# Performance work log

Measured on AMD Instinct MI355X. Metric: run time of the kernel, lower is better.

Reference implementation:

```python
import math
import jax, jax.numpy as jnp
import numpy as np

B, S, D, H = 8, 4096, 1024, 16
HD = D // H  # head_dim = 64


def setup_inputs() -> dict:
    key = jax.random.key(0)
    ks = jax.random.split(key, 13)
    sc = 1.0 / math.sqrt(D)
    scd = 1.0 / math.sqrt(HD)
    return {
        "X":   jax.random.normal(ks[0], (B, S, D), jnp.float32),
        "Wq":  jax.random.normal(ks[1], (D, D), jnp.float32) * sc,
        "bq":  jax.random.normal(ks[2], (D,), jnp.float32) * 0.01,
        "Wk":  jax.random.normal(ks[3], (D, D), jnp.float32) * sc,
        "bk":  jax.random.normal(ks[4], (D,), jnp.float32) * 0.01,
        "Wv":  jax.random.normal(ks[5], (D, D), jnp.float32) * sc,
        "bv":  jax.random.normal(ks[6], (D,), jnp.float32) * 0.01,
        "wql": jax.random.normal(ks[7], (HD,), jnp.float32) * scd,
        "bql": jax.random.normal(ks[8], (1,), jnp.float32) * 0.01,
        "wkl": jax.random.normal(ks[9], (HD,), jnp.float32) * scd,
        "bkl": jax.random.normal(ks[10], (1,), jnp.float32) * 0.01,
        "Wr":  jax.random.normal(ks[11], (HD, HD), jnp.float32) * scd,
        "br":  jax.random.normal(ks[12], (HD,), jnp.float32) * 0.01,
    }


def _split_heads(t):
    b, s, d = t.shape
    return t.reshape(b, s, H, HD).transpose(0, 2, 1, 3)  # b h s d


def reference(X, Wq, bq, Wk, bk, Wv, bv, wql, bql, wkl, bkl, Wr, br):
    inv_sqrt_d = 1.0 / math.sqrt(HD)
    q = _split_heads(X @ Wq + bq)  # [b,h,s,d]
    k = _split_heads(X @ Wk + bk)
    v = _split_heads(X @ Wv + bv)

    # query pooling: softmax over seq of a scalar logit per position
    alphas = jax.nn.softmax((jnp.einsum('bhsd,d->bhs', q, wql) + bql[0]) * inv_sqrt_d, axis=-1)
    global_query = jnp.einsum('bhs,bhsd->bhd', alphas, q)[:, :, None, :]  # [b,h,1,d]

    p = k * global_query  # elementwise gating, [b,h,s,d]
    betas = jax.nn.softmax((jnp.einsum('bhsd,d->bhs', p, wkl) + bkl[0]) * inv_sqrt_d, axis=-1)
    global_key = jnp.einsum('bhs,bhsd->bhd', betas, p)[:, :, None, :]  # [b,h,1,d]

    u = v * global_key  # [b,h,s,d]
    out = q + (u @ Wr + br)  # residual + tiny head_dim projection (dropout=0)
    b, h, s, d = out.shape
    return out.transpose(0, 2, 1, 3).reshape(b, s, h * d)
```

## Files before the change

### kernel.cpp

```cpp
#include <hip/hip_runtime.h>
#include <stdint.h>

#define B_   8
#define S_   4096
#define D_   1024
#define H_   16
#define HD_  64
#define M_   (B_ * S_)
#define N3   (3 * D_)

using f32x4 = __attribute__((ext_vector_type(4))) float;
using s8v   = __attribute__((ext_vector_type(8))) short;
using u16x8 = __attribute__((ext_vector_type(8))) unsigned short;
using bf8v  = __attribute__((ext_vector_type(8))) __bf16;

static __device__ __forceinline__ float bf2f(unsigned short u) {
  union { unsigned int i; float f; } x; x.i = ((unsigned int)u) << 16; return x.f;
}
static __device__ __forceinline__ unsigned short f2bf(float f) {
  union { float f; unsigned int i; } x; x.f = f;
  unsigned int r = x.i + 0x7fffu + ((x.i >> 16) & 1u);
  return (unsigned short)(r >> 16);
}

template <typename T>
static __device__ __forceinline__ auto mfma_try(T a, T b, f32x4 c, int)
    -> decltype(__builtin_amdgcn_mfma_f32_16x16x32_bf16(a, b, c, 0, 0, 0)) {
  return __builtin_amdgcn_mfma_f32_16x16x32_bf16(a, b, c, 0, 0, 0);
}
template <typename T>
static __device__ __forceinline__ f32x4 mfma_try(T a, T b, f32x4 c, long) {
  return __builtin_amdgcn_mfma_f32_16x16x32_bf16(
      __builtin_bit_cast(bf8v, a), __builtin_bit_cast(bf8v, b), c, 0, 0, 0);
}
static __device__ __forceinline__ f32x4 mfma_bf16(s8v a, s8v b, f32x4 c) {
  return mfma_try(a, b, c, 0);
}

static __device__ __forceinline__ void gl_lds16(const void* g, void* l) {
  __builtin_amdgcn_global_load_lds(
      (const __attribute__((address_space(1))) void*)g,
      (__attribute__((address_space(3))) void*)l, 16, 0, 0);
}

__global__ __launch_bounds__(256) void cvt_bf16_k(const float* __restrict__ in,
                                                  unsigned short* __restrict__ out) {
  size_t i = ((size_t)blockIdx.x * 256 + threadIdx.x) * 8;
  f32x4 a = *(const f32x4*)(in + i);
  f32x4 b = *(const f32x4*)(in + i + 4);
  u16x8 o;
#pragma unroll
  for (int j = 0; j < 4; ++j) { o[j] = f2bf(a[j]); o[4 + j] = f2bf(b[j]); }
  *(u16x8*)(out + i) = o;
}

__global__ __launch_bounds__(256) void packWT_k(const float* __restrict__ Wq,
                                                const float* __restrict__ Wk,
                                                const float* __restrict__ Wv,
                                                unsigned short* __restrict__ WT) {
  __shared__ unsigned short tile[64][65];
  const float* W = blockIdx.z == 0 ? Wq : (blockIdx.z == 1 ? Wk : Wv);
  unsigned short* O = WT + (size_t)blockIdx.z * 1024 * 1024;
  const int tk = blockIdx.x * 64, tn = blockIdx.y * 64;
  const int t = threadIdx.x;
#pragma unroll
  for (int i = 0; i < 16; ++i) {
    int idx = i * 256 + t; int r = idx >> 6, c = idx & 63;
    tile[c][r] = f2bf(W[(size_t)(tk + r) * 1024 + tn + c]);
  }
  __syncthreads();
#pragma unroll
  for (int i = 0; i < 16; ++i) {
    int idx = i * 256 + t; int r = idx >> 6, c = idx & 63;
    O[(size_t)(tn + r) * 1024 + tk + c] = tile[r][c];
  }
}

__global__ void packbias_k(const float* __restrict__ bq, const float* __restrict__ bk,
                           const float* __restrict__ bv, float* __restrict__ bcat) {
  int i = blockIdx.x * 256 + threadIdx.x;
  if (i < 1024) bcat[i] = bq[i];
  else if (i < 2048) bcat[i] = bk[i - 1024];
  else if (i < 3072) bcat[i] = bv[i - 2048];
}

__global__ __launch_bounds__(256) void gemm_qkv(const unsigned short* __restrict__ A,
                                                const unsigned short* __restrict__ BT,
                                                const float* __restrict__ bias,
                                                unsigned short* __restrict__ C) {
  __shared__ unsigned short As[128 * 64];
  __shared__ unsigned short Bs[128 * 64];
  const int t = threadIdx.x;
  const int w = t >> 6, l = t & 63;
  const int mrow0 = blockIdx.y * 128;
  const int ncol0 = blockIdx.x * 128;
  const int srow = t >> 3;
  const int scol = (t & 7) * 8;
  const unsigned short* Ag = A + (size_t)(mrow0 + srow) * 1024 + scol;
  const unsigned short* Bg = BT + (size_t)(ncol0 + srow) * 1024 + scol;
  unsigned short* Al = &As[srow * 64 + scol];
  unsigned short* Bl = &Bs[srow * 64 + scol];

  f32x4 acc[4][4];
#pragma unroll
  for (int m = 0; m < 4; ++m)
#pragma unroll
    for (int n = 0; n < 4; ++n) acc[m][n] = f32x4{0.f, 0.f, 0.f, 0.f};

  const int wr = (w >> 1) * 64, wc = (w & 1) * 64;
  const int fr = l & 15, fk = (l >> 4) * 8;

  for (int kt = 0; kt < 16; ++kt) {
    const int kk = kt * 64;
#pragma unroll
    for (int i = 0; i < 4; ++i) {
      gl_lds16(Ag + (size_t)(i * 32) * 1024 + kk, Al + i * 32 * 64);
      gl_lds16(Bg + (size_t)(i * 32) * 1024 + kk, Bl + i * 32 * 64);
    }
    __syncthreads();
#pragma unroll
    for (int ks = 0; ks < 2; ++ks) {
      s8v af[4], bf[4];
#pragma unroll
      for (int m = 0; m < 4; ++m)
        af[m] = *(const s8v*)&As[(wr + m * 16 + fr) * 64 + ks * 32 + fk];
#pragma unroll
      for (int n = 0; n < 4; ++n)
        bf[n] = *(const s8v*)&Bs[(wc + n * 16 + fr) * 64 + ks * 32 + fk];
#pragma unroll
      for (int m = 0; m < 4; ++m)
#pragma unroll
        for (int n = 0; n < 4; ++n)
          acc[m][n] = mfma_bf16(af[m], bf[n], acc[m][n]);
    }
    __syncthreads();
  }
  const int r4 = (l >> 4) * 4;
#pragma unroll
  for (int n = 0; n < 4; ++n) {
    const int gc = ncol0 + wc + n * 16 + fr;
    const float bb = bias[gc];
#pragma unroll
    for (int m = 0; m < 4; ++m)
#pragma unroll
      for (int i = 0; i < 4; ++i) {
        const int gr = mrow0 + wr + m * 16 + r4 + i;
        C[(size_t)gr * N3 + gc] = f2bf(acc[m][n][i] + bb);
      }
  }
}

template <int GATED>
__global__ __launch_bounds__(256) void plog_k(const unsigned short* __restrict__ QKV,
                                              const float* __restrict__ wvec,
                                              const float* __restrict__ bias,
                                              float* __restrict__ L, int off) {
  const int t = threadIdx.x;
  const int rg = blockIdx.x * 4 + (t >> 6);
  const int l = t & 63;
  const size_t base = (size_t)rg * N3 + off;
  u16x8 v0 = *(const u16x8*)(QKV + base + l * 16);
  u16x8 v1 = *(const u16x8*)(QKV + base + l * 16 + 8);
  const int h = l >> 2;
  const float* w;
  if (GATED) w = wvec + (((size_t)(rg >> 12) * 16 + h) * 64) + (l & 3) * 16;
  else       w = wvec + (l & 3) * 16;
  float d = 0.f;
#pragma unroll
  for (int j = 0; j < 8; ++j) d += bf2f(v0[j]) * w[j];
#pragma unroll
  for (int j = 0; j < 8; ++j) d += bf2f(v1[j]) * w[8 + j];
  d += __shfl_xor(d, 1); d += __shfl_xor(d, 2);
  if ((l & 3) == 0) L[(size_t)rg * 16 + h] = (d + bias[0]) * 0.125f;
}

__global__ __launch_bounds__(256) void pstats_k(const float* __restrict__ L,
                                                float* __restrict__ stats) {
  __shared__ float redm[4], reds[4];
  const int t = threadIdx.x;
  const int bh = blockIdx.x;
  const int b = bh >> 4, h = bh & 15;
  float vals[16];
  float mx = -1e30f;
#pragma unroll
  for (int j = 0; j < 16; ++j) {
    vals[j] = L[((size_t)b * S_ + t + j * 256) * 16 + h];
    mx = fmaxf(mx, vals[j]);
  }
  for (int off = 32; off; off >>= 1) mx = fmaxf(mx, __shfl_xor(mx, off));
  if ((t & 63) == 0) redm[t >> 6] = mx;
  __syncthreads();
  mx = fmaxf(fmaxf(redm[0], redm[1]), fmaxf(redm[2], redm[3]));
  float sm = 0.f;
#pragma unroll
  for (int j = 0; j < 16; ++j) sm += expf(vals[j] - mx);
  for (int off = 32; off; off >>= 1) sm += __shfl_xor(sm, off);
  if ((t & 63) == 0) reds[t >> 6] = sm;
  __syncthreads();
  if (t == 0) {
    stats[bh * 2] = mx;
    stats[bh * 2 + 1] = 1.f / (reds[0] + reds[1] + reds[2] + reds[3]);
  }
}

__global__ __launch_bounds__(256) void psum_k(const unsigned short* __restrict__ QKV,
                                              const float* __restrict__ L,
                                              const float* __restrict__ stats,
                                              float* __restrict__ pg, int off) {
  __shared__ float red2[256];
  const int t = threadIdx.x;
  const int c = blockIdx.x, bh = blockIdx.y;
  const int b = bh >> 4, h = bh & 15;
  const float MX = stats[bh * 2], INV = stats[bh * 2 + 1];
  const int w = t >> 6, d = t & 63;
  float acc = 0.f;
  const int s0 = c * 256 + w * 64;
#pragma unroll 4
  for (int i = 0; i < 64; ++i) {
    const size_t row = (size_t)b * S_ + s0 + i;
    const float a = expf(L[row * 16 + h] - MX) * INV;
    acc += a * bf2f(QKV[row * N3 + off + h * 64 + d]);
  }
  red2[t] = acc;
  __syncthreads();
  if (t < 64)
    pg[((size_t)bh * 16 + c) * 64 + t] =
        red2[t] + red2[64 + t] + red2[128 + t] + red2[192 + t];
}

__global__ __launch_bounds__(256) void predq_k(const float* __restrict__ pg,
                                               const float* __restrict__ wkl,
                                               float* __restrict__ gq,
                                               float* __restrict__ weffK) {
  const int idx = blockIdx.x * 256 + threadIdx.x;
  const int bh = idx >> 6, d = idx & 63;
  float s = 0.f;
#pragma unroll
  for (int c = 0; c < 16; ++c) s += pg[((size_t)bh * 16 + c) * 64 + d];
  gq[idx] = s;
  weffK[idx] = s * wkl[d];
}

__global__ __launch_bounds__(256) void predk_k(const float* __restrict__ pg,
                                               const float* __restrict__ gq,
                                               float* __restrict__ gk) {
  const int idx = blockIdx.x * 256 + threadIdx.x;
  const int bh = idx >> 6, d = idx & 63;
  float s = 0.f;
#pragma unroll
  for (int c = 0; c < 16; ++c) s += pg[((size_t)bh * 16 + c) * 64 + d];
  gk[idx] = gq[idx] * s;
}

__global__ __launch_bounds__(256) void final_out(const unsigned short* __restrict__ QKV,
                                                 const float* __restrict__ gk,
                                                 const float* __restrict__ Wr,
                                                 const float* __restrict__ br,
                                                 float* __restrict__ out) {
  __shared__ unsigned short Us[128 * 64];
  __shared__ float wrs[64 * 64];
  __shared__ float gks[64];
  const int t = threadIdx.x;
  const int w = t >> 6, l = t & 63;
  const int bh = blockIdx.y, sc = blockIdx.x;
  const int b = bh >> 4, h = bh & 15;
  const int s0 = sc * 128;
  if (t < 64) gks[t] = gk[bh * 64 + t];
#pragma unroll
  for (int i = 0; i < 16; ++i) wrs[i * 256 + t] = Wr[i * 256 + t];
  __syncthreads();
  const int rsub = t >> 3, csub = (t & 7) * 8;
  const size_t vbase = (((size_t)b * S_ + s0) * N3) + 2048 + h * 64;
#pragma unroll
  for (int i = 0; i < 4; ++i) {
    int r = i * 32 + rsub;
    u16x8 v = *(const u16x8*)(QKV + vbase + (size_t)r * N3 + csub);
    u16x8 u;
#pragma unroll
    for (int j = 0; j < 8; ++j) u[j] = f2bf(bf2f(v[j]) * gks[csub + j]);
    *(u16x8*)&Us[r * 64 + csub] = u;
  }
  const int fr = l & 15, fk = (l >> 4) * 8;
  s8v bfrag[2][4];
#pragma unroll
  for (int ks = 0; ks < 2; ++ks)
#pragma unroll
    for (int nf = 0; nf < 4; ++nf) {
      s8v tmp;
#pragma unroll
      for (int j = 0; j < 8; ++j)
        tmp[j] = (short)f2bf(wrs[(ks * 32 + fk + j) * 64 + nf * 16 + fr]);
      bfrag[ks][nf] = tmp;
    }
  __syncthreads();
  f32x4 acc[2][4];
#pragma unroll
  for (int rf = 0; rf < 2; ++rf)
#pragma unroll
    for (int nf = 0; nf < 4; ++nf) acc[rf][nf] = f32x4{0.f, 0.f, 0.f, 0.f};
#pragma unroll
  for (int ks = 0; ks < 2; ++ks) {
    s8v af[2];
#pragma unroll
    for (int rf = 0; rf < 2; ++rf)
      af[rf] = *(const s8v*)&Us[(w * 32 + rf * 16 + fr) * 64 + ks * 32 + fk];
#pragma unroll
    for (int rf = 0; rf < 2; ++rf)
#pragma unroll
      for (int nf = 0; nf < 4; ++nf)
        acc[rf][nf] = mfma_bf16(af[rf], bfrag[ks][nf], acc[rf][nf]);
  }
  const int r4 = (l >> 4) * 4;
#pragma unroll
  for (int rf = 0; rf < 2; ++rf)
#pragma unroll
    for (int nf = 0; nf < 4; ++nf)
#pragma unroll
      for (int i = 0; i < 4; ++i) {
        int srow = s0 + w * 32 + rf * 16 + r4 + i;
        int dcol = nf * 16 + fr;
        size_t row = (size_t)b * S_ + srow;
        float q = bf2f(QKV[row * N3 + h * 64 + dcol]);
        out[row * 1024 + h * 64 + dcol] = q + acc[rf][nf][i] + br[dcol];
      }
}

extern "C" void kernel_launch(void* const* d_in, const int* in_sizes, int n_in,
                              void* d_out, int out_size, void* d_ws, size_t ws_size,
                              hipStream_t stream) {
  const float* X   = (const float*)d_in[0];
  const float* Wq  = (const float*)d_in[1];
  const float* bq  = (const float*)d_in[2];
  const float* Wk  = (const float*)d_in[3];
  const float* bk  = (const float*)d_in[4];
  const float* Wv  = (const float*)d_in[5];
  const float* bv  = (const float*)d_in[6];
  const float* wql = (const float*)d_in[7];
  const float* bql = (const float*)d_in[8];
  const float* wkl = (const float*)d_in[9];
  const float* bkl = (const float*)d_in[10];
  const float* Wr  = (const float*)d_in[11];
  const float* br  = (const float*)d_in[12];
  float* out = (float*)d_out;

  char* ws = (char*)d_ws;
  unsigned short* Xb  = (unsigned short*)ws;
  unsigned short* WT  = (unsigned short*)(ws + 67108864);
  float* bcat         = (float*)(ws + 73400320);
  unsigned short* QKV = (unsigned short*)(ws + 73412608);
  float* Lq    = (float*)(ws + 0);
  float* Lk    = (float*)(ws + 2097152);
  float* pgq   = (float*)(ws + 4194304);
  float* pgk   = (float*)(ws + 4718592);
  float* statsQ= (float*)(ws + 5242880);
  float* statsK= (float*)(ws + 5246976);
  float* gq    = (float*)(ws + 6291456);
  float* weffK = (float*)(ws + 6324224);
  float* gk    = (float*)(ws + 6356992);

  hipLaunchKernelGGL(cvt_bf16_k, dim3(16384), dim3(256), 0, stream, X, Xb);
  hipLaunchKernelGGL(packWT_k, dim3(16, 16, 3), dim3(256), 0, stream, Wq, Wk, Wv, WT);
  hipLaunchKernelGGL(packbias_k, dim3(12), dim3(256), 0, stream, bq, bk, bv, bcat);
  hipLaunchKernelGGL(gemm_qkv, dim3(24, 256), dim3(256), 0, stream, Xb, WT, bcat, QKV);

  hipLaunchKernelGGL((plog_k<0>), dim3(8192), dim3(256), 0, stream, QKV, wql, bql, Lq, 0);
  hipLaunchKernelGGL(pstats_k, dim3(128), dim3(256), 0, stream, Lq, statsQ);
  hipLaunchKernelGGL(psum_k, dim3(16, 128), dim3(256), 0, stream, QKV, Lq, statsQ, pgq, 0);
  hipLaunchKernelGGL(predq_k, dim3(32), dim3(256), 0, stream, pgq, wkl, gq, weffK);
  hipLaunchKernelGGL((plog_k<1>), dim3(8192), dim3(256), 0, stream, QKV, weffK, bkl, Lk, 1024);
  hipLaunchKernelGGL(pstats_k, dim3(128), dim3(256), 0, stream, Lk, statsK);
  hipLaunchKernelGGL(psum_k, dim3(16, 128), dim3(256), 0, stream, QKV, Lk, statsK, pgk, 1024);
  hipLaunchKernelGGL(predk_k, dim3(32), dim3(256), 0, stream, pgk, gq, gk);

  hipLaunchKernelGGL(final_out, dim3(32, 128), dim3(256), 0, stream, QKV, gk, Wr, br, out);
}
```

Measured before the change: 659.1 us.

## Replace QKV GEMM with 256x256-tile double-buffered pipelined kernel

Swaps the 128x128-tile QKV GEMM for a 512-thread kernel that computes 256x256 tiles. It double-buffers 128KB of dynamic LDS so the next k-tile's global-to-LDS loads overlap the MFMA work, and uses an XOR swizzle to avoid LDS bank conflicts. It also remaps block IDs for better L2 locality and raises wave priority around the MFMAs. The aim is to raise arithmetic intensity and hide load latency, at the cost of more registers and LDS per block, which limits occupancy to one block per CU (128KB of 160KB), and more delicate hand-placed waitcnt/barrier synchronisation.

```diff
diff --git a/kernel.cpp b/kernel.cpp
--- a/kernel.cpp
+++ b/kernel.cpp
@@ -84,67 +84,116 @@
   else if (i < 3072) bcat[i] = bv[i - 2048];
 }
 
-__global__ __launch_bounds__(256) void gemm_qkv(const unsigned short* __restrict__ A,
-                                                const unsigned short* __restrict__ BT,
-                                                const float* __restrict__ bias,
-                                                unsigned short* __restrict__ C) {
-  __shared__ unsigned short As[128 * 64];
-  __shared__ unsigned short Bs[128 * 64];
+static __device__ __forceinline__ void stage_half(const unsigned short* __restrict__ g,
+                                                  int grow0, int ktile, int kh,
+                                                  char* lds_region, int t) {
+#pragma unroll
+  for (int j = 0; j < 2; ++j) {
+    const int li = j * 512 + t;
+    const int row = li >> 2, p = li & 3;
+    const int sg = kh * 4 + (p ^ (row & 3));
+    const unsigned short* src = g + (size_t)(grow0 + row) * 1024 + ktile * 64 + sg * 8;
+    gl_lds16(src, lds_region + kh * 16384 + li * 16);
+  }
+}
+
+__global__ __launch_bounds__(512, 2) void gemm256(const unsigned short* __restrict__ A,
+                                                  const unsigned short* __restrict__ BT,
+                                                  const float* __restrict__ bias,
+                                                  unsigned short* __restrict__ C) {
+  extern __shared__ char smem[];
   const int t = threadIdx.x;
   const int w = t >> 6, l = t & 63;
-  const int mrow0 = blockIdx.y * 128;
-  const int ncol0 = blockIdx.x * 128;
-  const int srow = t >> 3;
-  const int scol = (t & 7) * 8;
-  const unsigned short* Ag = A + (size_t)(mrow0 + srow) * 1024 + scol;
-  const unsigned short* Bg = BT + (size_t)(ncol0 + srow) * 1024 + scol;
-  unsigned short* Al = &As[srow * 64 + scol];
-  unsigned short* Bl = &Bs[srow * 64 + scol];
-
-  f32x4 acc[4][4];
-#pragma unroll
-  for (int m = 0; m < 4; ++m)
+  int bid = blockIdx.x;
+  const int cpx = gridDim.x >> 3;
+  bid = (bid & 7) * cpx + (bid >> 3);
+  const int by = bid & 127;
+  const int bx = bid >> 7;
+  const int mrow0 = by * 256, ncol0 = bx * 256;
+  const int wr = w >> 2, wc = w & 3;
+  const int fr = l & 15;
+  const int p_read = (((l >> 4) ^ (fr & 3)) << 4);
+
+  f32x4 acc[8][4];
+#pragma unroll
+  for (int m = 0; m < 8; ++m)
 #pragma unroll
     for (int n = 0; n < 4; ++n) acc[m][n] = f32x4{0.f, 0.f, 0.f, 0.f};
 
-  const int wr = (w >> 1) * 64, wc = (w & 1) * 64;
-  const int fr = l & 15, fk = (l >> 4) * 8;
-
-  for (int kt = 0; kt < 16; ++kt) {
-    const int kk = kt * 64;
-#pragma unroll
-    for (int i = 0; i < 4; ++i) {
-      gl_lds16(Ag + (size_t)(i * 32) * 1024 + kk, Al + i * 32 * 64);
-      gl_lds16(Bg + (size_t)(i * 32) * 1024 + kk, Bl + i * 32 * 64);
+  stage_half(A,  mrow0, 0, 0, smem, t);
+  stage_half(BT, ncol0, 0, 0, smem + 32768, t);
+  stage_half(A,  mrow0, 0, 1, smem, t);
+  stage_half(BT, ncol0, 0, 1, smem + 32768, t);
+  asm volatile("s_waitcnt vmcnt(4)" ::: "memory");
+  __builtin_amdgcn_s_barrier();
+  __builtin_amdgcn_sched_barrier(0);
+
+  const int arow = wr * 128 + fr;
+  const int brow = wc * 64 + fr;
+
+  for (int kt = 0; kt < 15; ++kt) {
+    const int base_rd = (kt & 1) * 65536;
+    const int base_wr = base_rd ^ 65536;
+#pragma unroll
+    for (int kk = 0; kk < 2; ++kk) {
+      s8v af[8], bfv[4];
+#pragma unroll
+      for (int m = 0; m < 8; ++m)
+        af[m] = *(const s8v*)(smem + base_rd + kk * 16384 + (arow + m * 16) * 64 + p_read);
+#pragma unroll
+      for (int n = 0; n < 4; ++n)
+        bfv[n] = *(const s8v*)(smem + base_rd + 32768 + kk * 16384 + (brow + n * 16) * 64 + p_read);
+      stage_half(A,  mrow0, kt + 1, kk, smem + base_wr, t);
+      stage_half(BT, ncol0, kt + 1, kk, smem + base_wr + 32768, t);
+      __builtin_amdgcn_s_setprio(1);
+#pragma unroll
+      for (int m = 0; m < 8; ++m)
+#pragma unroll
+        for (int n = 0; n < 4; ++n)
+          acc[m][n] = mfma_bf16(af[m], bfv[n], acc[m][n]);
+      __builtin_amdgcn_s_setprio(0);
+      __builtin_amdgcn_sched_barrier(0);
+      asm volatile("s_waitcnt vmcnt(4)" ::: "memory");
+      __builtin_amdgcn_s_barrier();
+      __builtin_amdgcn_sched_barrier(0);
     }
-    __syncthreads();
-#pragma unroll
-    for (int ks = 0; ks < 2; ++ks) {
-      s8v af[4], bf[4];
-#pragma unroll
-      for (int m = 0; m < 4; ++m)
-        af[m] = *(const s8v*)&As[(wr + m * 16 + fr) * 64 + ks * 32 + fk];
+  }
+  {
+    const int base_rd = 65536;
+#pragma unroll
+    for (int kk = 0; kk < 2; ++kk) {
+      s8v af[8], bfv[4];
+#pragma unroll
+      for (int m = 0; m < 8; ++m)
+        af[m] = *(const s8v*)(smem + base_rd + kk * 16384 + (arow + m * 16) * 64 + p_read);
 #pragma unroll
       for (int n = 0; n < 4; ++n)
-        bf[n] = *(const s8v*)&Bs[(wc + n * 16 + fr) * 64 + ks * 32 + fk];
-#pragma unroll
-      for (int m = 0; m < 4; ++m)
+        bfv[n] = *(const s8v*)(smem + base_rd + 32768 + kk * 16384 + (brow + n * 16) * 64 + p_read);
+      __builtin_amdgcn_s_setprio(1);
+#pragma unroll
+      for (int m = 0; m < 8; ++m)
 #pragma unroll
         for (int n = 0; n < 4; ++n)
-          acc[m][n] = mfma_bf16(af[m], bf[n], acc[m][n]);
+          acc[m][n] = mfma_bf16(af[m], bfv[n], acc[m][n]);
+      __builtin_amdgcn_s_setprio(0);
+      if (kk == 0) {
+        __builtin_amdgcn_sched_barrier(0);
+        asm volatile("s_waitcnt vmcnt(0)" ::: "memory");
+        __builtin_amdgcn_s_barrier();
+        __builtin_amdgcn_sched_barrier(0);
+      }
     }
-    __syncthreads();
   }
   const int r4 = (l >> 4) * 4;
 #pragma unroll
   for (int n = 0; n < 4; ++n) {
-    const int gc = ncol0 + wc + n * 16 + fr;
+    const int gc = ncol0 + wc * 64 + n * 16 + fr;
     const float bb = bias[gc];
 #pragma unroll
-    for (int m = 0; m < 4; ++m)
+    for (int m = 0; m < 8; ++m)
 #pragma unroll
       for (int i = 0; i < 4; ++i) {
-        const int gr = mrow0 + wr + m * 16 + r4 + i;
+        const int gr = mrow0 + wr * 128 + m * 16 + r4 + i;
         C[(size_t)gr * N3 + gc] = f2bf(acc[m][n][i] + bb);
       }
   }
@@ -358,10 +407,13 @@
   float* weffK = (float*)(ws + 6324224);
   float* gk    = (float*)(ws + 6356992);
 
+  hipFuncSetAttribute(reinterpret_cast<const void*>(gemm256),
+                      hipFuncAttributeMaxDynamicSharedMemorySize, 131072);
+
   hipLaunchKernelGGL(cvt_bf16_k, dim3(16384), dim3(256), 0, stream, X, Xb);
   hipLaunchKernelGGL(packWT_k, dim3(16, 16, 3), dim3(256), 0, stream, Wq, Wk, Wv, WT);
   hipLaunchKernelGGL(packbias_k, dim3(12), dim3(256), 0, stream, bq, bk, bv, bcat);
-  hipLaunchKernelGGL(gemm_qkv, dim3(24, 256), dim3(256), 0, stream, Xb, WT, bcat, QKV);
+  hipLaunchKernelGGL(gemm256, dim3(1536), dim3(512), 131072, stream, Xb, WT, bcat, QKV);
 
   hipLaunchKernelGGL((plog_k<0>), dim3(8192), dim3(256), 0, stream, QKV, wql, bql, Lq, 0);
   hipLaunchKernelGGL(pstats_k, dim3(128), dim3(256), 0, stream, Lq, statsQ);
```

New measurement: 624.0 us. 5.3% less time.

## Rewrite QKV GEMM as double-buffered 256x256 tile kernel and fuse softmax stats

Applied to the files above, without the earlier changes.

Replaces the 128x128 single-buffered QKV GEMM with a 256x256-tile, 512-thread kernel. It double-buffers 128 KB of dynamic LDS, interleaves global-to-LDS staging with MFMA quarter-steps using vmcnt waits and barriers, and remaps block IDs so neighbouring blocks reuse tiles in cache. The aim is to hide memory latency and raise data reuse in the dominant GEMM. Separately, the pstats kernel is folded into psum, so each psum block recomputes the softmax max and sum itself and two launches disappear, at the cost of redundant reduction work.

```diff
diff --git a/kernel.cpp b/kernel.cpp
--- a/kernel.cpp
+++ b/kernel.cpp
@@ -84,70 +84,130 @@
   else if (i < 3072) bcat[i] = bv[i - 2048];
 }
 
-__global__ __launch_bounds__(256) void gemm_qkv(const unsigned short* __restrict__ A,
-                                                const unsigned short* __restrict__ BT,
-                                                const float* __restrict__ bias,
-                                                unsigned short* __restrict__ C) {
-  __shared__ unsigned short As[128 * 64];
-  __shared__ unsigned short Bs[128 * 64];
+static __device__ __forceinline__ void stage_half(const unsigned short* __restrict__ g,
+                                                  int grow0, int kt, int h,
+                                                  char* region, int t) {
+#pragma unroll
+  for (int j = 0; j < 2; ++j) {
+    const int li = j * 512 + t;
+    const int kh = li >> 9, idx = li & 511;
+    const int row = h * 128 + (idx >> 2), slot = idx & 3;
+    const unsigned short* src = g + (size_t)(grow0 + row) * 1024 + kt * 64 + kh * 32 + slot * 8;
+    gl_lds16(src, region + kh * 16384 + h * 8192 + idx * 16);
+  }
+}
+
+#define VMCNT(n) asm volatile("s_waitcnt vmcnt(" #n ")" ::: "memory")
+#define BAR()    { __builtin_amdgcn_s_barrier(); __builtin_amdgcn_sched_barrier(0); }
+
+__global__ __launch_bounds__(512, 2) void gemm256(const unsigned short* __restrict__ A,
+                                                  const unsigned short* __restrict__ BT,
+                                                  const float* __restrict__ bias,
+                                                  unsigned short* __restrict__ C) {
+  extern __shared__ char smem[];
   const int t = threadIdx.x;
   const int w = t >> 6, l = t & 63;
-  const int mrow0 = blockIdx.y * 128;
-  const int ncol0 = blockIdx.x * 128;
-  const int srow = t >> 3;
-  const int scol = (t & 7) * 8;
-  const unsigned short* Ag = A + (size_t)(mrow0 + srow) * 1024 + scol;
-  const unsigned short* Bg = BT + (size_t)(ncol0 + srow) * 1024 + scol;
-  unsigned short* Al = &As[srow * 64 + scol];
-  unsigned short* Bl = &Bs[srow * 64 + scol];
-
-  f32x4 acc[4][4];
-#pragma unroll
-  for (int m = 0; m < 4; ++m)
+  const int cpx = gridDim.x >> 3;
+  const int lid = ((int)blockIdx.x & 7) * cpx + ((int)blockIdx.x >> 3);
+  const int by = lid / 12, bx = lid - by * 12;
+  const int mrow0 = by * 256, ncol0 = bx * 256;
+  const int wr = w >> 2, wc = w & 3;
+  const int fr = l & 15;
+  const int pr = (l >> 4) * 16;
+  const int arow0 = wr * 64 + fr;
+  const int brow0 = wc * 32 + fr;
+
+  f32x4 acc[8][4];
+#pragma unroll
+  for (int m = 0; m < 8; ++m)
 #pragma unroll
     for (int n = 0; n < 4; ++n) acc[m][n] = f32x4{0.f, 0.f, 0.f, 0.f};
 
-  const int wr = (w >> 1) * 64, wc = (w & 1) * 64;
-  const int fr = l & 15, fk = (l >> 4) * 8;
-
-  for (int kt = 0; kt < 16; ++kt) {
-    const int kk = kt * 64;
-#pragma unroll
-    for (int i = 0; i < 4; ++i) {
-      gl_lds16(Ag + (size_t)(i * 32) * 1024 + kk, Al + i * 32 * 64);
-      gl_lds16(Bg + (size_t)(i * 32) * 1024 + kk, Bl + i * 32 * 64);
-    }
-    __syncthreads();
-#pragma unroll
-    for (int ks = 0; ks < 2; ++ks) {
-      s8v af[4], bf[4];
-#pragma unroll
-      for (int m = 0; m < 4; ++m)
-        af[m] = *(const s8v*)&As[(wr + m * 16 + fr) * 64 + ks * 32 + fk];
-#pragma unroll
-      for (int n = 0; n < 4; ++n)
-        bf[n] = *(const s8v*)&Bs[(wc + n * 16 + fr) * 64 + ks * 32 + fk];
-#pragma unroll
-      for (int m = 0; m < 4; ++m)
-#pragma unroll
-        for (int n = 0; n < 4; ++n)
-          acc[m][n] = mfma_bf16(af[m], bf[n], acc[m][n]);
-    }
-    __syncthreads();
+  stage_half(A,  mrow0, 0, 0, smem, t);
+  stage_half(BT, ncol0, 0, 0, smem + 32768, t);
+  stage_half(BT, ncol0, 0, 1, smem + 32768, t);
+  stage_half(A,  mrow0, 0, 1, smem, t);
+  VMCNT(4);
+  BAR();
+
+  s8v a0[8], a1[8], b0[4], b1[4];
+
+#define RD_A(dst, MH, bufp)                                                        \
+  _Pragma("unroll") for (int mf = 0; mf < 4; ++mf)                                 \
+  _Pragma("unroll") for (int ks = 0; ks < 2; ++ks)                                 \
+    dst[mf * 2 + ks] = *(const s8v*)((bufp) + ks * 16384 +                         \
+                        ((MH) * 128 + arow0 + mf * 16) * 64 + pr);
+#define RD_B(dst, NH, bufp)                                                        \
+  _Pragma("unroll") for (int nf = 0; nf < 2; ++nf)                                 \
+  _Pragma("unroll") for (int ks = 0; ks < 2; ++ks)                                 \
+    dst[nf * 2 + ks] = *(const s8v*)((bufp) + 32768 + ks * 16384 +                 \
+                        ((NH) * 128 + brow0 + nf * 16) * 64 + pr);
+#define MFMA_Q(av, bv, MH, NH)                                                     \
+  __builtin_amdgcn_s_setprio(1);                                                   \
+  _Pragma("unroll") for (int mf = 0; mf < 4; ++mf)                                 \
+  _Pragma("unroll") for (int nf = 0; nf < 2; ++nf)                                 \
+  _Pragma("unroll") for (int ks = 0; ks < 2; ++ks)                                 \
+    acc[(MH) * 4 + mf][(NH) * 2 + nf] =                                            \
+        mfma_bf16(av[mf * 2 + ks], bv[nf * 2 + ks], acc[(MH) * 4 + mf][(NH) * 2 + nf]); \
+  __builtin_amdgcn_s_setprio(0);                                                   \
+  __builtin_amdgcn_sched_barrier(0);
+
+  for (int kt = 0; kt < 15; ++kt) {
+    char* buf  = smem + (kt & 1) * 65536;
+    char* nbuf = smem + ((kt + 1) & 1) * 65536;
+    RD_A(a0, 0, buf); RD_B(b0, 0, buf);
+    stage_half(A, mrow0, kt + 1, 0, nbuf, t);
+    BAR();
+    MFMA_Q(a0, b0, 0, 0);
+    VMCNT(4); BAR();
+    RD_B(b1, 1, buf);
+    stage_half(BT, ncol0, kt + 1, 0, nbuf + 32768, t);
+    BAR();
+    MFMA_Q(a0, b1, 0, 1);
+    VMCNT(4); BAR();
+    RD_A(a1, 1, buf);
+    stage_half(BT, ncol0, kt + 1, 1, nbuf + 32768, t);
+    BAR();
+    MFMA_Q(a1, b1, 1, 1);
+    VMCNT(4); BAR();
+    stage_half(A, mrow0, kt + 1, 1, nbuf, t);
+    BAR();
+    MFMA_Q(a1, b0, 1, 0);
+    VMCNT(4); BAR();
+  }
+  {
+    char* buf = smem + 65536;
+    RD_A(a0, 0, buf); RD_B(b0, 0, buf);
+    BAR();
+    MFMA_Q(a0, b0, 0, 0);
+    VMCNT(2); BAR();
+    RD_B(b1, 1, buf);
+    BAR();
+    MFMA_Q(a0, b1, 0, 1);
+    VMCNT(0); BAR();
+    RD_A(a1, 1, buf);
+    MFMA_Q(a1, b1, 1, 1);
+    MFMA_Q(a1, b0, 1, 0);
   }
   const int r4 = (l >> 4) * 4;
 #pragma unroll
-  for (int n = 0; n < 4; ++n) {
-    const int gc = ncol0 + wc + n * 16 + fr;
-    const float bb = bias[gc];
-#pragma unroll
-    for (int m = 0; m < 4; ++m)
-#pragma unroll
-      for (int i = 0; i < 4; ++i) {
-        const int gr = mrow0 + wr + m * 16 + r4 + i;
-        C[(size_t)gr * N3 + gc] = f2bf(acc[m][n][i] + bb);
-      }
-  }
+  for (int mh = 0; mh < 2; ++mh)
+#pragma unroll
+    for (int mf = 0; mf < 4; ++mf)
+#pragma unroll
+      for (int nh = 0; nh < 2; ++nh)
+#pragma unroll
+        for (int nf = 0; nf < 2; ++nf) {
+          const int gc = ncol0 + nh * 128 + wc * 32 + nf * 16 + fr;
+          const int grb = mrow0 + mh * 128 + wr * 64 + mf * 16 + r4;
+          const float bb = bias[gc];
+#pragma unroll
+          for (int i = 0; i < 4; ++i)
+            C[(size_t)(grb + i) * N3 + gc] = f2bf(acc[mh * 4 + mf][nh * 2 + nf][i] + bb);
+        }
+#undef RD_A
+#undef RD_B
+#undef MFMA_Q
 }
 
 template <int GATED>
@@ -174,11 +234,12 @@
   if ((l & 3) == 0) L[(size_t)rg * 16 + h] = (d + bias[0]) * 0.125f;
 }
 
-__global__ __launch_bounds__(256) void pstats_k(const float* __restrict__ L,
-                                                float* __restrict__ stats) {
-  __shared__ float redm[4], reds[4];
+__global__ __launch_bounds__(256) void psum_k(const unsigned short* __restrict__ QKV,
+                                              const float* __restrict__ L,
+                                              float* __restrict__ pg, int off) {
+  __shared__ float redm[4], reds[4], red2[256];
   const int t = threadIdx.x;
-  const int bh = blockIdx.x;
+  const int c = blockIdx.x, bh = blockIdx.y;
   const int b = bh >> 4, h = bh & 15;
   float vals[16];
   float mx = -1e30f;
@@ -187,31 +248,18 @@
     vals[j] = L[((size_t)b * S_ + t + j * 256) * 16 + h];
     mx = fmaxf(mx, vals[j]);
   }
-  for (int off = 32; off; off >>= 1) mx = fmaxf(mx, __shfl_xor(mx, off));
+  for (int off2 = 32; off2; off2 >>= 1) mx = fmaxf(mx, __shfl_xor(mx, off2));
   if ((t & 63) == 0) redm[t >> 6] = mx;
   __syncthreads();
   mx = fmaxf(fmaxf(redm[0], redm[1]), fmaxf(redm[2], redm[3]));
   float sm = 0.f;
 #pragma unroll
   for (int j = 0; j < 16; ++j) sm += expf(vals[j] - mx);
-  for (int off = 32; off; off >>= 1) sm += __shfl_xor(sm, off);
+  for (int off2 = 32; off2; off2 >>= 1) sm += __shfl_xor(sm, off2);
   if ((t & 63) == 0) reds[t >> 6] = sm;
   __syncthreads();
-  if (t == 0) {
-    stats[bh * 2] = mx;
-    stats[bh * 2 + 1] = 1.f / (reds[0] + reds[1] + reds[2] + reds[3]);
-  }
-}
-
-__global__ __launch_bounds__(256) void psum_k(const unsigned short* __restrict__ QKV,
-                                              const float* __restrict__ L,
-                                              const float* __restrict__ stats,
-                                              float* __restrict__ pg, int off) {
-  __shared__ float red2[256];
-  const int t = threadIdx.x;
-  const int c = blockIdx.x, bh = blockIdx.y;
-  const int b = bh >> 4, h = bh & 15;
-  const float MX = stats[bh * 2], INV = stats[bh * 2 + 1];
+  const float MX = mx;
+  const float INV = 1.f / (reds[0] + reds[1] + reds[2] + reds[3]);
   const int w = t >> 6, d = t & 63;
   float acc = 0.f;
   const int s0 = c * 256 + w * 64;
@@ -352,24 +400,23 @@
   float* Lk    = (float*)(ws + 2097152);
   float* pgq   = (float*)(ws + 4194304);
   float* pgk   = (float*)(ws + 4718592);
-  float* statsQ= (float*)(ws + 5242880);
-  float* statsK= (float*)(ws + 5246976);
   float* gq    = (float*)(ws + 6291456);
   float* weffK = (float*)(ws + 6324224);
   float* gk    = (float*)(ws + 6356992);
 
+  hipFuncSetAttribute(reinterpret_cast<const void*>(gemm256),
+                      hipFuncAttributeMaxDynamicSharedMemorySize, 131072);
+
   hipLaunchKernelGGL(cvt_bf16_k, dim3(16384), dim3(256), 0, stream, X, Xb);
   hipLaunchKernelGGL(packWT_k, dim3(16, 16, 3), dim3(256), 0, stream, Wq, Wk, Wv, WT);
   hipLaunchKernelGGL(packbias_k, dim3(12), dim3(256), 0, stream, bq, bk, bv, bcat);
-  hipLaunchKernelGGL(gemm_qkv, dim3(24, 256), dim3(256), 0, stream, Xb, WT, bcat, QKV);
+  hipLaunchKernelGGL(gemm256, dim3(1536), dim3(512), 131072, stream, Xb, WT, bcat, QKV);
 
   hipLaunchKernelGGL((plog_k<0>), dim3(8192), dim3(256), 0, stream, QKV, wql, bql, Lq, 0);
-  hipLaunchKernelGGL(pstats_k, dim3(128), dim3(256), 0, stream, Lq, statsQ);
-  hipLaunchKernelGGL(psum_k, dim3(16, 128), dim3(256), 0, stream, QKV, Lq, statsQ, pgq, 0);
+  hipLaunchKernelGGL(psum_k, dim3(16, 128), dim3(256), 0, stream, QKV, Lq, pgq, 0);
   hipLaunchKernelGGL(predq_k, dim3(32), dim3(256), 0, stream, pgq, wkl, gq, weffK);
   hipLaunchKernelGGL((plog_k<1>), dim3(8192), dim3(256), 0, stream, QKV, weffK, bkl, Lk, 1024);
-  hipLaunchKernelGGL(pstats_k, dim3(128), dim3(256), 0, stream, Lk, statsK);
-  hipLaunchKernelGGL(psum_k, dim3(16, 128), dim3(256), 0, stream, QKV, Lk, statsK, pgk, 1024);
+  hipLaunchKernelGGL(psum_k, dim3(16, 128), dim3(256), 0, stream, QKV, Lk, pgk, 1024);
   hipLaunchKernelGGL(predk_k, dim3(32), dim3(256), 0, stream, pgk, gq, gk);
 
   hipLaunchKernelGGL(final_out, dim3(32, 128), dim3(256), 0, stream, QKV, gk, Wr, br, out);
```

New measurement: 601.5 us. 1.1x faster.
